# Optimization experiments

Hardware: AMD Instinct MI355X
Metric: run time of the kernel (lower is better)

Reference implementation:

```python
import jax, jax.numpy as jnp
import numpy as np

B, LQ, LK = 8, 256, 256
Q_SIZE = K_SIZE = H = D_V = 256
MASK_VALUE = -1000000.0


def setup_inputs() -> dict:
    key = jax.random.key(0)
    kq, kk, kv, kl, kwq, kwk, kwv = jax.random.split(key, 7)
    # Linear weights, torch nn.Linear stores (out, in); init ~ U(-1/sqrt(in), 1/sqrt(in))
    def lin(k, out_f, in_f):
        bound = 1.0 / np.sqrt(in_f)
        return jax.random.uniform(k, (out_f, in_f), jnp.float32, -bound, bound)
    return {
        "queries": jax.random.normal(kq, (B, LQ, Q_SIZE), jnp.float32),
        "keyes": jax.random.normal(kk, (B, LK, K_SIZE), jnp.float32),
        "values": jax.random.normal(kv, (B, LK, D_V), jnp.float32),
        "valid_lens": jax.random.randint(kl, (B,), 1, LK + 1),
        "W_q": lin(kwq, H, Q_SIZE),
        "W_k": lin(kwk, H, K_SIZE),
        "W_v": lin(kwv, 1, H),
    }


def reference(queries, keyes, values, valid_lens, W_q, W_k, W_v):
    # Projections (nn.Linear without bias): x @ W.T
    q = jnp.einsum("bqd,hd->bqh", queries, W_q)            # (B, Lq, H)
    k = jnp.einsum("bkd,hd->bkh", keyes, W_k)              # (B, Lk, H)
    # Broadcast-add + tanh: (B, Lq, Lk, H)
    features = jnp.tanh(q[:, :, None, :] + k[:, None, :, :])
    # W_v reduction H -> 1, squeeze: scores (B, Lq, Lk)
    scores = jnp.einsum("bqkh,h->bqk", features, W_v[0])
    # sequence_mask over the last (key) axis with value -1e6
    lk = scores.shape[-1]
    mask = jnp.arange(lk)[None, None, :] < valid_lens[:, None, None]  # (B,1,Lk)
    scores = jnp.where(mask, scores, MASK_VALUE)
    # NOTE: this repo's masked_softmax normalizes over dim=1 (the query axis),
    # faithfully reproduced here.
    attention_weights = jax.nn.softmax(scores, axis=1)
    # dropout is identity in eval / p=0.0
    return jnp.einsum("bqk,bkd->bqd", attention_weights, values)
```

## Files before the change

### kernel.cpp

```cpp
#include <hip/hip_runtime.h>

typedef float vf4 __attribute__((ext_vector_type(4)));

#define LOG2E 1.4426950408889634f
#define TWO_LOG2E 2.8853900817779268f

__device__ __forceinline__ float fexp2(float x) { return __builtin_amdgcn_exp2f(x); }
__device__ __forceinline__ float frcp(float x) { return __builtin_amdgcn_rcpf(x); }

__global__ __launch_bounds__(256) void proj_kernel(
    const float* __restrict__ queries, const float* __restrict__ keyes,
    const float* __restrict__ Wq, const float* __restrict__ Wk,
    float* __restrict__ QpH, float* __restrict__ KpH,
    float* __restrict__ Rsum) {
  __shared__ alignas(16) float At[16 * 68];
  __shared__ alignas(16) float Bt[16 * 68];
  const int t = threadIdx.x;
  if (blockIdx.x == 0 && blockIdx.y == 0 && blockIdx.z == 0) {
    *(vf4*)&Rsum[t * 8] = (vf4){0.f, 0.f, 0.f, 0.f};
    *(vf4*)&Rsum[t * 8 + 4] = (vf4){0.f, 0.f, 0.f, 0.f};
  }
  const int m0 = blockIdx.x * 64;
  const int n0 = blockIdx.y * 64;
  const int k0 = blockIdx.z * 128;
  const bool isQ = (m0 < 2048);
  const float* X = isQ ? queries : keyes;
  const float* W = isQ ? Wq : Wk;
  float* C = (isQ ? QpH : KpH) + blockIdx.z * 524288;
  const int mb = isQ ? m0 : (m0 - 2048);

  const int lm = t >> 2;
  const int lq = t & 3;
  const int mm4 = (t & 15) * 4;
  const int nn4 = (t >> 4) * 4;

  float acc[4][4] = {};
  for (int kc = k0; kc < k0 + 128; kc += 16) {
    __syncthreads();
    vf4 xa = *(const vf4*)&X[(mb + lm) * 256 + kc + lq * 4];
    vf4 wb = *(const vf4*)&W[(n0 + lm) * 256 + kc + lq * 4];
#pragma unroll
    for (int c = 0; c < 4; ++c) {
      At[(lq * 4 + c) * 68 + lm] = xa[c];
      Bt[(lq * 4 + c) * 68 + lm] = wb[c];
    }
    __syncthreads();
#pragma unroll
    for (int kk = 0; kk < 16; ++kk) {
      vf4 a4 = *(const vf4*)&At[kk * 68 + mm4];
      vf4 b4 = *(const vf4*)&Bt[kk * 68 + nn4];
#pragma unroll
      for (int i = 0; i < 4; ++i)
#pragma unroll
        for (int j = 0; j < 4; ++j) acc[i][j] += a4[i] * b4[j];
    }
  }
#pragma unroll
  for (int i = 0; i < 4; ++i) {
    vf4 o = {acc[i][0] * TWO_LOG2E, acc[i][1] * TWO_LOG2E,
             acc[i][2] * TWO_LOG2E, acc[i][3] * TWO_LOG2E};
    *(vf4*)&C[(mb + mm4 + i) * 256 + n0 + nn4] = o;
  }
}

__global__ __launch_bounds__(256) void scores_exp_kernel(
    const float* __restrict__ QpH, const float* __restrict__ KpH,
    const float* __restrict__ Wv, const int* __restrict__ valid_lens,
    float* __restrict__ E, float* __restrict__ Rsum) {
  __shared__ alignas(16) float Qs[32 * 32];
  __shared__ alignas(16) float Ks[32 * 32];
  __shared__ alignas(16) float wvs[256];
  const int t = threadIdx.x;
  const int i0 = blockIdx.x * 32;
  const int j0 = blockIdx.y * 32;
  const int b = blockIdx.z;
  const int ti = t & 15;
  const int tj = t >> 4;

  float Swv;
  {
    vf4 w4 = *(const vf4*)&Wv[(t & 63) * 4];
    float sw = w4[0] + w4[1] + w4[2] + w4[3];
#pragma unroll
    for (int off = 1; off < 64; off <<= 1) sw += __shfl_xor(sw, off, 64);
    Swv = sw;
  }
  if (t < 64) *(vf4*)&wvs[t * 4] = *(const vf4*)&Wv[t * 4];

  const int srow = t >> 3;
  const int scg = t & 7;
  const int swcol = ((scg ^ (srow & 7)) << 2);
  const int qxor = ti & 7;
  const int kxor = tj & 7;

  float acc[2][2] = {};
  for (int hc = 0; hc < 8; ++hc) {
    __syncthreads();
    const int qoff = (((b << 8) + i0 + srow) << 8) + hc * 32 + scg * 4;
    const int koff = (((b << 8) + j0 + srow) << 8) + hc * 32 + scg * 4;
    vf4 qv = *(const vf4*)&QpH[qoff];
    vf4 qv2 = *(const vf4*)&QpH[524288 + qoff];
    vf4 kv = *(const vf4*)&KpH[koff];
    vf4 kv2 = *(const vf4*)&KpH[524288 + koff];
    *(vf4*)&Qs[srow * 32 + swcol] = qv + qv2;
    *(vf4*)&Ks[srow * 32 + swcol] = kv + kv2;
    __syncthreads();
#pragma unroll
    for (int hh = 0; hh < 8; ++hh) {
      vf4 q0 = *(const vf4*)&Qs[ti * 32 + ((hh ^ qxor) << 2)];
      vf4 q1 = *(const vf4*)&Qs[(ti + 16) * 32 + ((hh ^ qxor) << 2)];
      vf4 k0 = *(const vf4*)&Ks[tj * 32 + ((hh ^ kxor) << 2)];
      vf4 k1 = *(const vf4*)&Ks[(tj + 16) * 32 + ((hh ^ kxor) << 2)];
      vf4 wv4 = *(const vf4*)&wvs[hc * 32 + hh * 4];
#pragma unroll
      for (int e = 0; e < 4; ++e) {
        const float we = wv4[e];
        acc[0][0] += we * frcp(fexp2(q0[e] + k0[e]) + 1.0f);
        acc[0][1] += we * frcp(fexp2(q0[e] + k1[e]) + 1.0f);
        acc[1][0] += we * frcp(fexp2(q1[e] + k0[e]) + 1.0f);
        acc[1][1] += we * frcp(fexp2(q1[e] + k1[e]) + 1.0f);
      }
    }
  }

  const int len = valid_lens[b];
#pragma unroll
  for (int c = 0; c < 2; ++c) {
    const int j = j0 + tj + 16 * c;
    const bool masked = (j >= len);
    float ev[2];
#pragma unroll
    for (int r = 0; r < 2; ++r) {
      const int i = i0 + ti + 16 * r;
      const float score = Swv - 2.0f * acc[r][c];
      ev[r] = masked ? 1.0f : fexp2(score * LOG2E);
      E[(((b << 8) + j) << 8) + i] = ev[r];
    }
    float s = ev[0] + ev[1];
#pragma unroll
    for (int off = 1; off < 16; off <<= 1) s += __shfl_xor(s, off, 64);
    if (ti == 0) atomicAdd(&Rsum[(b << 8) + j], s);
  }
}

__global__ __launch_bounds__(128) void out_kernel(
    const float* __restrict__ E, const float* __restrict__ Rsum,
    const float* __restrict__ V, float* __restrict__ out) {
  __shared__ alignas(16) float As[32 * 36];
  __shared__ alignas(16) float Bs[32 * 68];
  const int t = threadIdx.x;
  const int i0 = blockIdx.x * 32;
  const int d0 = blockIdx.y * 64;
  const int b = blockIdx.z;
  const int ti = t & 7;
  const int td = t >> 3;
  const int srow = t >> 2;
  const int scg = t & 3;

  float acc[4][4] = {};
  for (int jc = 0; jc < 8; ++jc) {
    const int jb = jc * 32;
    __syncthreads();
    const float rj = frcp(Rsum[(b << 8) + jb + srow]);
#pragma unroll
    for (int s = 0; s < 2; ++s) {
      const int col = scg * 8 + s * 4;
      vf4 a = *(const vf4*)&E[(((b << 8) + jb + srow) << 8) + i0 + col];
      *(vf4*)&As[srow * 36 + col] = a * rj;
    }
#pragma unroll
    for (int s = 0; s < 4; ++s) {
      const int col = scg * 16 + s * 4;
      *(vf4*)&Bs[srow * 68 + col] =
          *(const vf4*)&V[(((b << 8) + jb + srow) << 8) + d0 + col];
    }
    __syncthreads();
#pragma unroll
    for (int j = 0; j < 32; ++j) {
      vf4 a4 = *(const vf4*)&As[j * 36 + ti * 4];
      vf4 b4 = *(const vf4*)&Bs[j * 68 + td * 4];
#pragma unroll
      for (int r = 0; r < 4; ++r)
#pragma unroll
        for (int c = 0; c < 4; ++c) acc[r][c] += a4[r] * b4[c];
    }
  }
#pragma unroll
  for (int r = 0; r < 4; ++r) {
    vf4 o = {acc[r][0], acc[r][1], acc[r][2], acc[r][3]};
    *(vf4*)&out[(((b << 8) + i0 + ti * 4 + r) << 8) + d0 + td * 4] = o;
  }
}

extern "C" void kernel_launch(void* const* d_in, const int* in_sizes, int n_in,
                              void* d_out, int out_size, void* d_ws, size_t ws_size,
                              hipStream_t stream) {
  const float* queries = (const float*)d_in[0];
  const float* keyes = (const float*)d_in[1];
  const float* values = (const float*)d_in[2];
  const int* valid_lens = (const int*)d_in[3];
  const float* Wq = (const float*)d_in[4];
  const float* Wk = (const float*)d_in[5];
  const float* Wv = (const float*)d_in[6];
  float* out = (float*)d_out;

  float* QpH = (float*)d_ws;
  float* KpH = QpH + 2 * 524288;
  float* E = KpH + 2 * 524288;
  float* Rsum = E + 524288;

  proj_kernel<<<dim3(64, 4, 2), 256, 0, stream>>>(queries, keyes, Wq, Wk,
                                                  QpH, KpH, Rsum);
  scores_exp_kernel<<<dim3(8, 8, 8), 256, 0, stream>>>(QpH, KpH, Wv,
                                                       valid_lens, E, Rsum);
  out_kernel<<<dim3(8, 4, 8), 128, 0, stream>>>(E, Rsum, values, out);
}
```

Before: 125.4 us.

## Precompute exponentials of projections so scores use multiply instead of exp

The projection kernel now stores exp(2q) and exp(2k) instead of the scaled q and k. The split-K partial sums are combined by multiplication rather than addition, using exp(a+b)=exp(a)exp(b). This lets the scores inner loop compute 1/(1+eq*ek) with a single fma and rcp, removing the per-element exp2 over the B×Lq×Lk×H volume. The output GEMM kernel is also retiled to 256 threads with a 2x4 per-thread tile. Exponentiating first adds some risk of overflow or precision loss for large projection values.

```diff
diff --git a/kernel.cpp b/kernel.cpp
--- a/kernel.cpp
+++ b/kernel.cpp
@@ -57,8 +57,8 @@
   }
 #pragma unroll
   for (int i = 0; i < 4; ++i) {
-    vf4 o = {acc[i][0] * TWO_LOG2E, acc[i][1] * TWO_LOG2E,
-             acc[i][2] * TWO_LOG2E, acc[i][3] * TWO_LOG2E};
+    vf4 o = {fexp2(acc[i][0] * TWO_LOG2E), fexp2(acc[i][1] * TWO_LOG2E),
+             fexp2(acc[i][2] * TWO_LOG2E), fexp2(acc[i][3] * TWO_LOG2E)};
     *(vf4*)&C[(mb + mm4 + i) * 256 + n0 + nn4] = o;
   }
 }
@@ -102,8 +102,8 @@
     vf4 qv2 = *(const vf4*)&QpH[524288 + qoff];
     vf4 kv = *(const vf4*)&KpH[koff];
     vf4 kv2 = *(const vf4*)&KpH[524288 + koff];
-    *(vf4*)&Qs[srow * 32 + swcol] = qv + qv2;
-    *(vf4*)&Ks[srow * 32 + swcol] = kv + kv2;
+    *(vf4*)&Qs[srow * 32 + swcol] = qv * qv2;
+    *(vf4*)&Ks[srow * 32 + swcol] = kv * kv2;
     __syncthreads();
 #pragma unroll
     for (int hh = 0; hh < 8; ++hh) {
@@ -115,10 +115,10 @@
 #pragma unroll
       for (int e = 0; e < 4; ++e) {
         const float we = wv4[e];
-        acc[0][0] += we * frcp(fexp2(q0[e] + k0[e]) + 1.0f);
-        acc[0][1] += we * frcp(fexp2(q0[e] + k1[e]) + 1.0f);
-        acc[1][0] += we * frcp(fexp2(q1[e] + k0[e]) + 1.0f);
-        acc[1][1] += we * frcp(fexp2(q1[e] + k1[e]) + 1.0f);
+        acc[0][0] += we * frcp(__builtin_fmaf(q0[e], k0[e], 1.0f));
+        acc[0][1] += we * frcp(__builtin_fmaf(q0[e], k1[e], 1.0f));
+        acc[1][0] += we * frcp(__builtin_fmaf(q1[e], k0[e], 1.0f));
+        acc[1][1] += we * frcp(__builtin_fmaf(q1[e], k1[e], 1.0f));
       }
     }
   }
@@ -143,7 +143,7 @@
   }
 }
 
-__global__ __launch_bounds__(128) void out_kernel(
+__global__ __launch_bounds__(256) void out_kernel(
     const float* __restrict__ E, const float* __restrict__ Rsum,
     const float* __restrict__ V, float* __restrict__ out) {
   __shared__ alignas(16) float As[32 * 36];
@@ -152,43 +152,43 @@
   const int i0 = blockIdx.x * 32;
   const int d0 = blockIdx.y * 64;
   const int b = blockIdx.z;
-  const int ti = t & 7;
-  const int td = t >> 3;
-  const int srow = t >> 2;
-  const int scg = t & 3;
-
-  float acc[4][4] = {};
+  const int ti = t & 15;
+  const int td = t >> 4;
+  const int sr = t >> 3;
+  const int sc4 = (t & 7) * 4;
+
+  float acc[2][4] = {};
   for (int jc = 0; jc < 8; ++jc) {
     const int jb = jc * 32;
     __syncthreads();
-    const float rj = frcp(Rsum[(b << 8) + jb + srow]);
+    const float rj = frcp(Rsum[(b << 8) + jb + sr]);
+    {
+      vf4 a = *(const vf4*)&E[(((b << 8) + jb + sr) << 8) + i0 + sc4];
+      *(vf4*)&As[sr * 36 + sc4] = a * rj;
+    }
 #pragma unroll
     for (int s = 0; s < 2; ++s) {
-      const int col = scg * 8 + s * 4;
-      vf4 a = *(const vf4*)&E[(((b << 8) + jb + srow) << 8) + i0 + col];
-      *(vf4*)&As[srow * 36 + col] = a * rj;
-    }
-#pragma unroll
-    for (int s = 0; s < 4; ++s) {
-      const int col = scg * 16 + s * 4;
-      *(vf4*)&Bs[srow * 68 + col] =
-          *(const vf4*)&V[(((b << 8) + jb + srow) << 8) + d0 + col];
+      const int col = sc4 + s * 32;
+      *(vf4*)&Bs[sr * 68 + col] =
+          *(const vf4*)&V[(((b << 8) + jb + sr) << 8) + d0 + col];
     }
     __syncthreads();
 #pragma unroll
     for (int j = 0; j < 32; ++j) {
-      vf4 a4 = *(const vf4*)&As[j * 36 + ti * 4];
+      const float a0 = As[j * 36 + ti];
+      const float a1 = As[j * 36 + ti + 16];
       vf4 b4 = *(const vf4*)&Bs[j * 68 + td * 4];
 #pragma unroll
-      for (int r = 0; r < 4; ++r)
-#pragma unroll
-        for (int c = 0; c < 4; ++c) acc[r][c] += a4[r] * b4[c];
-    }
-  }
-#pragma unroll
-  for (int r = 0; r < 4; ++r) {
+      for (int c = 0; c < 4; ++c) {
+        acc[0][c] += a0 * b4[c];
+        acc[1][c] += a1 * b4[c];
+      }
+    }
+  }
+#pragma unroll
+  for (int r = 0; r < 2; ++r) {
     vf4 o = {acc[r][0], acc[r][1], acc[r][2], acc[r][3]};
-    *(vf4*)&out[(((b << 8) + i0 + ti * 4 + r) << 8) + d0 + td * 4] = o;
+    *(vf4*)&out[(((b << 8) + i0 + ti + 16 * r) << 8) + d0 + td * 4] = o;
   }
 }
 
@@ -213,5 +213,5 @@
                                                   QpH, KpH, Rsum);
   scores_exp_kernel<<<dim3(8, 8, 8), 256, 0, stream>>>(QpH, KpH, Wv,
                                                        valid_lens, E, Rsum);
-  out_kernel<<<dim3(8, 4, 8), 128, 0, stream>>>(E, Rsum, values, out);
-}
+  out_kernel<<<dim3(8, 4, 8), 256, 0, stream>>>(E, Rsum, values, out);
+}
```

New measurement: 111.5 us (median of 2 runs). -11.1%, faster.
